# Optimization experiments

Measured on AMD Instinct MI355X. Metric: run time of the kernel, lower is better.

## Reference

```python
import jax, jax.numpy as jnp
import numpy as np

B, T, C = 2, 2048, 1024
N_HEAD = 16
HEAD_DIM = C // N_HEAD


def setup_inputs() -> dict:
    key = jax.random.key(0)
    k1, k2, k3 = jax.random.split(key, 3)
    x = jax.random.normal(k1, (B, T, C), dtype=jnp.float32)
    # weights stored as [in, out]; torch Linear computes x @ W.T with weight [out, in]
    W_qkv = jax.random.normal(k2, (C, 3 * C), dtype=jnp.float32) * (1.0 / np.sqrt(C))
    W_proj = jax.random.normal(k3, (C, C), dtype=jnp.float32) * (1.0 / np.sqrt(C))
    return {"x": x, "W_qkv": W_qkv, "W_proj": W_proj}


def reference(x, W_qkv, W_proj):
    Bb, Tt, Cc = x.shape
    qkv = x @ W_qkv                                # [B,T,3C]
    q, k, v = jnp.split(qkv, 3, axis=2)
    # [B,T,H,D] -> [B,H,T,D]
    q = q.reshape(Bb, Tt, N_HEAD, HEAD_DIM).transpose(0, 2, 1, 3)
    k = k.reshape(Bb, Tt, N_HEAD, HEAD_DIM).transpose(0, 2, 1, 3)
    v = v.reshape(Bb, Tt, N_HEAD, HEAD_DIM).transpose(0, 2, 1, 3)
    scale = 1.0 / np.sqrt(HEAD_DIM).astype(np.float32)
    att = jnp.einsum('bhqd,bhkd->bhqk', q, k) * scale   # [B,H,T,T]
    causal = jnp.tril(jnp.ones((Tt, Tt), dtype=bool))
    att = jnp.where(causal[None, None], att, -jnp.inf)
    att = jax.nn.softmax(att, axis=-1)
    y = jnp.einsum('bhqk,bhkd->bhqd', att, v)           # [B,H,T,D]
    y = y.transpose(0, 2, 1, 3).reshape(Bb, Tt, Cc)
    return y @ W_proj
```

## Files before the change

### kernel.cpp

```cpp
#include <hip/hip_runtime.h>
#include <hip/hip_bf16.h>
#include <math.h>


typedef __bf16 bf16_t;
typedef __bf16 bf16x4 __attribute__((ext_vector_type(4)));
typedef __bf16 bf16x8 __attribute__((ext_vector_type(8)));
typedef float  f32x4  __attribute__((ext_vector_type(4)));
typedef unsigned int u32x4 __attribute__((ext_vector_type(4)));

#define MFMA16(a, b, c) __builtin_amdgcn_mfma_f32_16x16x32_bf16((a), (b), (c), 0, 0, 0)

#define Bn 2
#define Tn 2048
#define Cn 1024
#define Hn 16
#define Dn 64
#define C3 3072
#define Mn 4096
#define QKW 2048
#define NEG_BIG (-1e30f)
#define SCL2 0.18033688011112042f

__device__ __forceinline__ void gload_lds16(const void* g, void* l) {
    __builtin_amdgcn_global_load_lds(
        (const __attribute__((address_space(1))) unsigned int*)g,
        (__attribute__((address_space(3))) unsigned int*)l, 16, 0, 0);
}

__device__ __forceinline__ unsigned cvtpk_bf16(float a, float b) {
    unsigned r;
    asm("v_cvt_pk_bf16_f32 %0, %1, %2" : "=v"(r) : "v"(a), "v"(b));
    return r;
}

__global__ __launch_bounds__(256) void transpose_cvt(const float* __restrict__ in,
                                                     bf16_t* __restrict__ out,
                                                     int K, int N) {
    __shared__ float tile[32][33];
    int n0 = blockIdx.x * 32, k0 = blockIdx.y * 32;
    int tx = threadIdx.x, ty = threadIdx.y;
#pragma unroll
    for (int i = 0; i < 32; i += 8)
        tile[ty + i][tx] = in[(size_t)(k0 + ty + i) * N + n0 + tx];
    __syncthreads();
#pragma unroll
    for (int i = 0; i < 32; i += 8)
        out[(size_t)(n0 + ty + i) * K + k0 + tx] = (bf16_t)tile[tx][ty + i];
}

__global__ __launch_bounds__(256) void cvt_bf16(const float* __restrict__ in,
                                                bf16_t* __restrict__ out) {
    size_t i = ((size_t)blockIdx.x * 256 + threadIdx.x) * 8;
    f32x4 a = *(const f32x4*)(in + i);
    f32x4 b = *(const f32x4*)(in + i + 4);
    bf16x8 r;
    r[0] = (bf16_t)a[0]; r[1] = (bf16_t)a[1]; r[2] = (bf16_t)a[2]; r[3] = (bf16_t)a[3];
    r[4] = (bf16_t)b[0]; r[5] = (bf16_t)b[1]; r[6] = (bf16_t)b[2]; r[7] = (bf16_t)b[3];
    *(bf16x8*)(out + i) = r;
}

template <typename AT, typename CT, int MODE>
__global__ __launch_bounds__(256) void gemm_m97(const AT* __restrict__ A, int lda,
                                                const bf16_t* __restrict__ BT,
                                                CT* __restrict__ Cout, int ldc, int Kd,
                                                bf16_t* __restrict__ qk,
                                                bf16_t* __restrict__ vT) {
    constexpr bool AF32 = (sizeof(AT) == 4);
    __shared__ AT     As[128 * 32];
    __shared__ bf16_t Bs[128 * 32];

    const int tid = threadIdx.x;
    const int w = tid >> 6, lane = tid & 63;
    const int l16 = lane & 15, quad = lane >> 4;
    const int wm = w & 1, wn = w >> 1;
    const int n0 = blockIdx.x * 128;
    const int m0 = blockIdx.y * 128;

    f32x4 zero = {0.f, 0.f, 0.f, 0.f};
    f32x4 acc[4][4];
#pragma unroll
    for (int mb = 0; mb < 4; mb++)
#pragma unroll
        for (int nb = 0; nb < 4; nb++) acc[mb][nb] = zero;

    for (int k = 0; k < Kd; k += 32) {
        __syncthreads();
        if (AF32) {
#pragma unroll
            for (int j = 0; j < 4; j++) {
                int seg = w * 4 + j;
                int r = seg * 8 + (lane >> 3);
                int cc = (lane & 7) ^ (r & 7);
                const float* g = (const float*)A + (size_t)(m0 + r) * lda + k + cc * 4;
                gload_lds16(g, (char*)As + seg * 1024);
            }
        } else {
#pragma unroll
            for (int j = 0; j < 2; j++) {
                int seg = w * 2 + j;
                int r = seg * 16 + (lane >> 2);
                int cc = (lane & 3) ^ (r & 3);
                const bf16_t* g = (const bf16_t*)A + (size_t)(m0 + r) * lda + k + cc * 8;
                gload_lds16(g, (char*)As + seg * 1024);
            }
        }
#pragma unroll
        for (int j = 0; j < 2; j++) {
            int seg = w * 2 + j;
            int r = seg * 16 + (lane >> 2);
            int cc = (lane & 3) ^ (r & 3);
            const bf16_t* g = BT + (size_t)(n0 + r) * Kd + k + cc * 8;
            gload_lds16(g, (char*)Bs + seg * 1024);
        }
        __syncthreads();

        bf16x8 af[4], bf[4];
#pragma unroll
        for (int mb = 0; mb < 4; mb++) {
            int r = wm * 64 + mb * 16 + l16;
            if (AF32) {
                f32x4 x0 = *(const f32x4*)((const char*)As + (r * 8 + ((quad * 2) ^ (r & 7))) * 16);
                f32x4 x1 = *(const f32x4*)((const char*)As + (r * 8 + ((quad * 2 + 1) ^ (r & 7))) * 16);
                bf16x8 t;
                t[0] = (bf16_t)x0[0]; t[1] = (bf16_t)x0[1]; t[2] = (bf16_t)x0[2]; t[3] = (bf16_t)x0[3];
                t[4] = (bf16_t)x1[0]; t[5] = (bf16_t)x1[1]; t[6] = (bf16_t)x1[2]; t[7] = (bf16_t)x1[3];
                af[mb] = t;
            } else {
                af[mb] = *(const bf16x8*)((const char*)As + (r * 4 + (quad ^ (r & 3))) * 16);
            }
        }
#pragma unroll
        for (int nb = 0; nb < 4; nb++) {
            int r = wn * 64 + nb * 16 + l16;
            bf[nb] = *(const bf16x8*)((const char*)Bs + (r * 4 + (quad ^ (r & 3))) * 16);
        }
#pragma unroll
        for (int mb = 0; mb < 4; mb++)
#pragma unroll
            for (int nb = 0; nb < 4; nb++)
                acc[mb][nb] = MFMA16(af[mb], bf[nb], acc[mb][nb]);
    }

#pragma unroll
    for (int mb = 0; mb < 4; mb++)
#pragma unroll
        for (int nb = 0; nb < 4; nb++) {
            const int col = n0 + wn * 64 + nb * 16 + l16;
            const int row0 = m0 + wm * 64 + mb * 16 + quad * 4;
            if (MODE == 0) {
#pragma unroll
                for (int rr = 0; rr < 4; rr++)
                    Cout[(size_t)(row0 + rr) * ldc + col] = (CT)acc[mb][nb][rr];
            } else {
                if (col < 2048) {
                    const float sc = (col < 1024) ? SCL2 : 1.0f;
#pragma unroll
                    for (int rr = 0; rr < 4; rr++)
                        qk[(size_t)(row0 + rr) * QKW + col] = (bf16_t)(acc[mb][nb][rr] * sc);
                } else {
                    int hcol = col - 2048;
                    int bb = row0 >> 11, t0 = row0 & 2047;
                    bf16x4 pv;
#pragma unroll
                    for (int rr = 0; rr < 4; rr++) pv[rr] = (bf16_t)acc[mb][nb][rr];
                    *(bf16x4*)(vT + ((size_t)(bb * 1024 + hcol)) * Tn + t0) = pv;
                }
            }
        }
}

__global__ __launch_bounds__(256) void gemm_s(const bf16_t* __restrict__ A, int lda,
                                              const bf16_t* __restrict__ BT,
                                              float* __restrict__ Cout, int ldc, int Kd) {
    __shared__ bf16_t As[64 * 32];
    __shared__ bf16_t Bs[128 * 32];

    const int tid = threadIdx.x;
    const int w = tid >> 6, lane = tid & 63;
    const int l16 = lane & 15, quad = lane >> 4;
    const int wm = w & 1, wn = w >> 1;
    const int n0 = blockIdx.x * 128;
    const int m0 = blockIdx.y * 64;

    f32x4 zero = {0.f, 0.f, 0.f, 0.f};
    f32x4 acc[2][4];
#pragma unroll
    for (int mb = 0; mb < 2; mb++)
#pragma unroll
        for (int nb = 0; nb < 4; nb++) acc[mb][nb] = zero;

    for (int k = 0; k < Kd; k += 32) {
        __syncthreads();
        {
            int r = w * 16 + (lane >> 2);
            int cc = (lane & 3) ^ (r & 3);
            const bf16_t* g = A + (size_t)(m0 + r) * lda + k + cc * 8;
            gload_lds16(g, (char*)As + w * 1024);
        }
#pragma unroll
        for (int j = 0; j < 2; j++) {
            int seg = w * 2 + j;
            int r = seg * 16 + (lane >> 2);
            int cc = (lane & 3) ^ (r & 3);
            const bf16_t* g = BT + (size_t)(n0 + r) * Kd + k + cc * 8;
            gload_lds16(g, (char*)Bs + seg * 1024);
        }
        __syncthreads();

        bf16x8 af[2], bf[4];
#pragma unroll
        for (int mb = 0; mb < 2; mb++) {
            int r = wm * 32 + mb * 16 + l16;
            af[mb] = *(const bf16x8*)((const char*)As + (r * 4 + (quad ^ (r & 3))) * 16);
        }
#pragma unroll
        for (int nb = 0; nb < 4; nb++) {
            int r = wn * 64 + nb * 16 + l16;
            bf[nb] = *(const bf16x8*)((const char*)Bs + (r * 4 + (quad ^ (r & 3))) * 16);
        }
#pragma unroll
        for (int mb = 0; mb < 2; mb++)
#pragma unroll
            for (int nb = 0; nb < 4; nb++)
                acc[mb][nb] = MFMA16(af[mb], bf[nb], acc[mb][nb]);
    }

#pragma unroll
    for (int mb = 0; mb < 2; mb++)
#pragma unroll
        for (int nb = 0; nb < 4; nb++) {
            const int col = n0 + wn * 64 + nb * 16 + l16;
            const int row0 = m0 + wm * 32 + mb * 16 + quad * 4;
#pragma unroll
            for (int rr = 0; rr < 4; rr++)
                Cout[(size_t)(row0 + rr) * ldc + col] = acc[mb][nb][rr];
        }
}

__global__ __launch_bounds__(256) void attn_kernel(bf16_t* __restrict__ qk,
                                                   const bf16_t* __restrict__ vT) {
    const int id = blockIdx.x;
    const int bh = id & 31;
    const int pr = id >> 5;
    const int b = bh >> 4, h = bh & 15;
    const int tA = pr;
    const int tB = 31 - pr;
    const int tmax = tB;

    const int tid = threadIdx.x;
    const int wave = tid >> 6, lane = tid & 63;
    const int l16 = lane & 15, quad = lane >> 4;

    __shared__ __align__(16) bf16_t Kb[3][64 * 64];
    __shared__ __align__(16) bf16_t Vb[3][64 * 64];

    bf16_t* qbase = qk + (size_t)b * Tn * QKW + h * Dn;
    const bf16_t* kbase = qk + (size_t)b * Tn * QKW + Cn + h * Dn;
    const bf16_t* vbase = vT + (size_t)(b * 1024 + h * Dn) * Tn;

    const int qA = tA * 64 + wave * 16;
    const int qB = tB * 64 + wave * 16;

    bf16x8 qfA[2], qfB[2];
#pragma unroll
    for (int ks = 0; ks < 2; ks++) {
        qfA[ks] = *(const bf16x8*)(qbase + (size_t)(qA + l16) * QKW + ks * 32 + quad * 8);
        qfB[ks] = *(const bf16x8*)(qbase + (size_t)(qB + l16) * QKW + ks * 32 + quad * 8);
    }

    bf16x8 ones;
#pragma unroll
    for (int j = 0; j < 8; j++) ones[j] = (bf16_t)1.0f;

    f32x4 zero = {0.f, 0.f, 0.f, 0.f};
    f32x4 oA[4], oB[4];
    f32x4 olA, olB;
#pragma unroll
    for (int i = 0; i < 4; i++) { oA[i] = zero; oB[i] = zero; }
    olA = zero; olB = zero;

    const int gl = quad >> 1, sub = (quad & 1) * 8;
    int kOff[2][4], vLo[2][4], vHi[2][4];
#pragma unroll
    for (int ks = 0; ks < 2; ks++)
#pragma unroll
        for (int nb = 0; nb < 4; nb++) {
            int R = nb * 16 + l16, r7 = R & 7;
            kOff[ks][nb] = R * 128 + (((ks * 4 + quad) ^ r7) << 4);
            vLo[ks][nb]  = R * 128 + (((ks * 4 + gl) ^ r7) << 4) + sub;
            vHi[ks][nb]  = R * 128 + (((ks * 4 + 2 + gl) ^ r7) << 4) + sub;
        }

    const int r8 = lane >> 3;
    const int cc = (lane & 7) ^ r8;
    auto STAGE = [&](int t, int pg) {
        const int key0 = t * 64;
#pragma unroll
        for (int j = 0; j < 2; j++) {
            int seg = wave * 2 + j;
            gload_lds16(kbase + (size_t)(key0 + seg * 8 + r8) * QKW + cc * 8,
                        (char*)&Kb[pg][0] + seg * 1024);
            gload_lds16(vbase + (size_t)(seg * 8 + r8) * Tn + key0 + cc * 8,
                        (char*)&Vb[pg][0] + seg * 1024);
        }
    };

    STAGE(0, 0);
    STAGE(1, 1);
    int cur = 0;

    for (int t = 0; t <= tmax; ++t) {
        asm volatile("s_waitcnt vmcnt(4)" ::: "memory");
        __builtin_amdgcn_sched_barrier(0);
        __builtin_amdgcn_s_barrier();
        __builtin_amdgcn_sched_barrier(0);
        if (t + 2 <= tmax) {
            int st = cur + 2; if (st >= 3) st -= 3;
            STAGE(t + 2, st);
        }
        __builtin_amdgcn_sched_barrier(0);

        const bool shp = (t <= tA);
        const char* Kc = (const char*)&Kb[cur][0];
        const char* Vc = (const char*)&Vb[cur][0];

        bf16x8 kf[2][4];
#pragma unroll
        for (int ks = 0; ks < 2; ks++)
#pragma unroll
            for (int nbk = 0; nbk < 4; nbk++)
                kf[ks][nbk] = *(const bf16x8*)(Kc + kOff[ks][nbk]);

        bf16x8 pfA[2], pfB[2];

        {
            f32x4 sx[4];
#pragma unroll
            for (int nbk = 0; nbk < 4; nbk++) sx[nbk] = zero;
            __builtin_amdgcn_s_setprio(1);
#pragma unroll
            for (int nbk = 0; nbk < 4; nbk++) {
                sx[nbk] = MFMA16(kf[0][nbk], qfB[0], sx[nbk]);
                sx[nbk] = MFMA16(kf[1][nbk], qfB[1], sx[nbk]);
            }
            __builtin_amdgcn_s_setprio(0);
            if (t == tB) {
                int q = qB + l16;
#pragma unroll
                for (int nbk = 0; nbk < 4; nbk++)
#pragma unroll
                    for (int r = 0; r < 4; r++) {
                        int key = t * 64 + nbk * 16 + quad * 4 + r;
                        if (key > q) sx[nbk][r] = NEG_BIG;
                    }
            }
#pragma unroll
            for (int nbk = 0; nbk < 4; nbk++)
#pragma unroll
                for (int r = 0; r < 4; r++)
                    sx[nbk][r] = __builtin_amdgcn_exp2f(sx[nbk][r]);
#pragma unroll
            for (int ks = 0; ks < 2; ks++) {
                u32x4 wds;
                wds.x = cvtpk_bf16(sx[2 * ks][0], sx[2 * ks][1]);
                wds.y = cvtpk_bf16(sx[2 * ks][2], sx[2 * ks][3]);
                wds.z = cvtpk_bf16(sx[2 * ks + 1][0], sx[2 * ks + 1][1]);
                wds.w = cvtpk_bf16(sx[2 * ks + 1][2], sx[2 * ks + 1][3]);
                pfB[ks] = __builtin_bit_cast(bf16x8, wds);
            }
        }

        if (shp) {
            f32x4 sx[4];
#pragma unroll
            for (int nbk = 0; nbk < 4; nbk++) sx[nbk] = zero;
            __builtin_amdgcn_s_setprio(1);
#pragma unroll
            for (int nbk = 0; nbk < 4; nbk++) {
                sx[nbk] = MFMA16(kf[0][nbk], qfA[0], sx[nbk]);
                sx[nbk] = MFMA16(kf[1][nbk], qfA[1], sx[nbk]);
            }
            __builtin_amdgcn_s_setprio(0);
            if (t == tA) {
                int q = qA + l16;
#pragma unroll
                for (int nbk = 0; nbk < 4; nbk++)
#pragma unroll
                    for (int r = 0; r < 4; r++) {
                        int key = t * 64 + nbk * 16 + quad * 4 + r;
                        if (key > q) sx[nbk][r] = NEG_BIG;
                    }
            }
#pragma unroll
            for (int nbk = 0; nbk < 4; nbk++)
#pragma unroll
                for (int r = 0; r < 4; r++)
                    sx[nbk][r] = __builtin_amdgcn_exp2f(sx[nbk][r]);
#pragma unroll
            for (int ks = 0; ks < 2; ks++) {
                u32x4 wds;
                wds.x = cvtpk_bf16(sx[2 * ks][0], sx[2 * ks][1]);
                wds.y = cvtpk_bf16(sx[2 * ks][2], sx[2 * ks][3]);
                wds.z = cvtpk_bf16(sx[2 * ks + 1][0], sx[2 * ks + 1][1]);
                wds.w = cvtpk_bf16(sx[2 * ks + 1][2], sx[2 * ks + 1][3]);
                pfA[ks] = __builtin_bit_cast(bf16x8, wds);
            }
        } else {
            u32x4 z = {0u, 0u, 0u, 0u};
            pfA[0] = __builtin_bit_cast(bf16x8, z);
            pfA[1] = __builtin_bit_cast(bf16x8, z);
        }

        __builtin_amdgcn_s_setprio(1);
#pragma unroll
        for (int ks = 0; ks < 2; ks++) {
#pragma unroll
            for (int nbd = 0; nbd < 4; nbd++) {
                bf16x4 lo = *(const bf16x4*)(Vc + vLo[ks][nbd]);
                bf16x4 hi = *(const bf16x4*)(Vc + vHi[ks][nbd]);
                bf16x8 vf;
                vf[0] = lo[0]; vf[1] = lo[1]; vf[2] = lo[2]; vf[3] = lo[3];
                vf[4] = hi[0]; vf[5] = hi[1]; vf[6] = hi[2]; vf[7] = hi[3];
                oB[nbd] = MFMA16(pfB[ks], vf, oB[nbd]);
                if (shp) oA[nbd] = MFMA16(pfA[ks], vf, oA[nbd]);
            }
            olB = MFMA16(pfB[ks], ones, olB);
            if (shp) olA = MFMA16(pfA[ks], ones, olA);
        }
        __builtin_amdgcn_s_setprio(0);

        cur = cur + 1; if (cur >= 3) cur -= 3;
    }

#pragma unroll
    for (int nbd = 0; nbd < 4; nbd++)
#pragma unroll
        for (int r = 0; r < 4; r++) {
            int ta = qA + quad * 4 + r;
            int tb = qB + quad * 4 + r;
            qbase[(size_t)ta * QKW + nbd * 16 + l16] = (bf16_t)(oA[nbd][r] / olA[r]);
            qbase[(size_t)tb * QKW + nbd * 16 + l16] = (bf16_t)(oB[nbd][r] / olB[r]);
        }
}

extern "C" void kernel_launch(void* const* d_in, const int* in_sizes, int n_in,
                              void* d_out, int out_size, void* d_ws, size_t ws_size,
                              hipStream_t stream) {
    const float* x     = (const float*)d_in[0];
    const float* Wqkv  = (const float*)d_in[1];
    const float* Wproj = (const float*)d_in[2];
    float* out = (float*)d_out;

    bf16_t* qk     = (bf16_t*)d_ws;
    bf16_t* vT     = qk + (size_t)Mn * QKW;
    bf16_t* wqkvT  = vT + (size_t)QKW * Tn;
    bf16_t* wprojT = wqkvT + (size_t)C3 * Cn;
    bf16_t* xb     = wprojT + (size_t)Cn * Cn;

    const size_t NEED_XB = ((size_t)Mn * QKW + (size_t)QKW * Tn + (size_t)C3 * Cn +
                            (size_t)Cn * Cn + (size_t)Mn * Cn) * sizeof(bf16_t);

    transpose_cvt<<<dim3(C3 / 32, Cn / 32), dim3(32, 8), 0, stream>>>(Wqkv, wqkvT, Cn, C3);
    transpose_cvt<<<dim3(Cn / 32, Cn / 32), dim3(32, 8), 0, stream>>>(Wproj, wprojT, Cn, Cn);

    if (ws_size >= NEED_XB) {
        cvt_bf16<<<dim3((Mn * Cn) / 2048), 256, 0, stream>>>(x, xb);
        gemm_m97<bf16_t, bf16_t, 1><<<dim3(C3 / 128, Mn / 128), 256, 0, stream>>>(
            xb, Cn, wqkvT, (bf16_t*)nullptr, 0, Cn, qk, vT);
    } else {
        gemm_m97<float, bf16_t, 1><<<dim3(C3 / 128, Mn / 128), 256, 0, stream>>>(
            x, Cn, wqkvT, (bf16_t*)nullptr, 0, Cn, qk, vT);
    }
    attn_kernel<<<dim3(512), 256, 0, stream>>>(qk, vT);
    gemm_s<<<dim3(Cn / 128, Mn / 64), 256, 0, stream>>>(qk, QKW, wprojT, out, Cn, Cn);
}
```

Before: 187.5 us.

## Fuse prep kernels, stage V epilogue through LDS, and simplify V fragment loads

```diff
diff --git a/kernel.cpp b/kernel.cpp
--- a/kernel.cpp
+++ b/kernel.cpp
@@ -34,12 +34,35 @@
     return r;
 }
 
-__global__ __launch_bounds__(256) void transpose_cvt(const float* __restrict__ in,
-                                                     bf16_t* __restrict__ out,
-                                                     int K, int N) {
+__global__ __launch_bounds__(256) void prep(const float* __restrict__ Wqkv,
+                                            const float* __restrict__ Wproj,
+                                            const float* __restrict__ x,
+                                            bf16_t* __restrict__ wqkvT,
+                                            bf16_t* __restrict__ wprojT,
+                                            bf16_t* __restrict__ xb) {
     __shared__ float tile[32][33];
-    int n0 = blockIdx.x * 32, k0 = blockIdx.y * 32;
-    int tx = threadIdx.x, ty = threadIdx.y;
+    const int bid = blockIdx.x;
+    const int tid = threadIdx.x;
+    if (bid >= 4096) {
+        size_t i = ((size_t)(bid - 4096) * 256 + tid) * 8;
+        f32x4 a = *(const f32x4*)(x + i);
+        f32x4 b = *(const f32x4*)(x + i + 4);
+        bf16x8 r;
+        r[0] = (bf16_t)a[0]; r[1] = (bf16_t)a[1]; r[2] = (bf16_t)a[2]; r[3] = (bf16_t)a[3];
+        r[4] = (bf16_t)b[0]; r[5] = (bf16_t)b[1]; r[6] = (bf16_t)b[2]; r[7] = (bf16_t)b[3];
+        *(bf16x8*)(xb + i) = r;
+        return;
+    }
+    const float* in; bf16_t* out; int K, N, n0, k0;
+    if (bid < 3072) {
+        in = Wqkv; out = wqkvT; K = Cn; N = C3;
+        n0 = (bid % 96) * 32; k0 = (bid / 96) * 32;
+    } else {
+        int b2 = bid - 3072;
+        in = Wproj; out = wprojT; K = Cn; N = Cn;
+        n0 = (b2 & 31) * 32; k0 = (b2 >> 5) * 32;
+    }
+    const int tx = tid & 31, ty = tid >> 5;
 #pragma unroll
     for (int i = 0; i < 32; i += 8)
         tile[ty + i][tx] = in[(size_t)(k0 + ty + i) * N + n0 + tx];
@@ -47,17 +70,6 @@
 #pragma unroll
     for (int i = 0; i < 32; i += 8)
         out[(size_t)(n0 + ty + i) * K + k0 + tx] = (bf16_t)tile[tx][ty + i];
-}
-
-__global__ __launch_bounds__(256) void cvt_bf16(const float* __restrict__ in,
-                                                bf16_t* __restrict__ out) {
-    size_t i = ((size_t)blockIdx.x * 256 + threadIdx.x) * 8;
-    f32x4 a = *(const f32x4*)(in + i);
-    f32x4 b = *(const f32x4*)(in + i + 4);
-    bf16x8 r;
-    r[0] = (bf16_t)a[0]; r[1] = (bf16_t)a[1]; r[2] = (bf16_t)a[2]; r[3] = (bf16_t)a[3];
-    r[4] = (bf16_t)b[0]; r[5] = (bf16_t)b[1]; r[6] = (bf16_t)b[2]; r[7] = (bf16_t)b[3];
-    *(bf16x8*)(out + i) = r;
 }
 
 template <typename AT, typename CT, int MODE>
@@ -67,8 +79,12 @@
                                                 bf16_t* __restrict__ qk,
                                                 bf16_t* __restrict__ vT) {
     constexpr bool AF32 = (sizeof(AT) == 4);
-    __shared__ AT     As[128 * 32];
-    __shared__ bf16_t Bs[128 * 32];
+    constexpr int SZ_AB = 128 * 32 * (int)sizeof(AT) + 128 * 32 * (int)sizeof(bf16_t);
+    constexpr int SZ_VS = 128 * 136 * (int)sizeof(bf16_t);
+    constexpr int SZ = (MODE == 1 && SZ_VS > SZ_AB) ? SZ_VS : SZ_AB;
+    __shared__ __align__(16) char smem[SZ];
+    AT*     As = (AT*)smem;
+    bf16_t* Bs = (bf16_t*)(smem + 128 * 32 * sizeof(AT));
 
     const int tid = threadIdx.x;
     const int w = tid >> 6, lane = tid & 63;
@@ -142,32 +158,53 @@
                 acc[mb][nb] = MFMA16(af[mb], bf[nb], acc[mb][nb]);
     }
 
-#pragma unroll
-    for (int mb = 0; mb < 4; mb++)
-#pragma unroll
-        for (int nb = 0; nb < 4; nb++) {
-            const int col = n0 + wn * 64 + nb * 16 + l16;
-            const int row0 = m0 + wm * 64 + mb * 16 + quad * 4;
-            if (MODE == 0) {
+    if (MODE == 0) {
+#pragma unroll
+        for (int mb = 0; mb < 4; mb++)
+#pragma unroll
+            for (int nb = 0; nb < 4; nb++) {
+                const int col = n0 + wn * 64 + nb * 16 + l16;
+                const int row0 = m0 + wm * 64 + mb * 16 + quad * 4;
 #pragma unroll
                 for (int rr = 0; rr < 4; rr++)
                     Cout[(size_t)(row0 + rr) * ldc + col] = (CT)acc[mb][nb][rr];
-            } else {
-                if (col < 2048) {
-                    const float sc = (col < 1024) ? SCL2 : 1.0f;
-#pragma unroll
-                    for (int rr = 0; rr < 4; rr++)
-                        qk[(size_t)(row0 + rr) * QKW + col] = (bf16_t)(acc[mb][nb][rr] * sc);
-                } else {
-                    int hcol = col - 2048;
-                    int bb = row0 >> 11, t0 = row0 & 2047;
-                    bf16x4 pv;
-#pragma unroll
-                    for (int rr = 0; rr < 4; rr++) pv[rr] = (bf16_t)acc[mb][nb][rr];
-                    *(bf16x4*)(vT + ((size_t)(bb * 1024 + hcol)) * Tn + t0) = pv;
-                }
-            }
-        }
+            }
+    } else if (n0 < 2048) {
+#pragma unroll
+        for (int mb = 0; mb < 4; mb++)
+#pragma unroll
+            for (int nb = 0; nb < 4; nb++) {
+                const int col = n0 + wn * 64 + nb * 16 + l16;
+                const int row0 = m0 + wm * 64 + mb * 16 + quad * 4;
+                const float sc = (col < 1024) ? SCL2 : 1.0f;
+#pragma unroll
+                for (int rr = 0; rr < 4; rr++)
+                    qk[(size_t)(row0 + rr) * QKW + col] = (bf16_t)(acc[mb][nb][rr] * sc);
+            }
+    } else {
+        __syncthreads();
+        bf16_t* vs = (bf16_t*)smem;
+#pragma unroll
+        for (int mb = 0; mb < 4; mb++)
+#pragma unroll
+            for (int nb = 0; nb < 4; nb++) {
+                int lcol = wn * 64 + nb * 16 + l16;
+                int lrow = wm * 64 + mb * 16 + quad * 4;
+                int lr = (lrow & ~31) | (((lrow >> 2) & 3) << 3) | (((lrow >> 4) & 1) << 2);
+                bf16x4 pv;
+#pragma unroll
+                for (int rr = 0; rr < 4; rr++) pv[rr] = (bf16_t)acc[mb][nb][rr];
+                *(bf16x4*)(vs + lcol * 136 + lr) = pv;
+            }
+        __syncthreads();
+        const int hc = tid >> 1, hf = (tid & 1) * 64;
+        const int bb = m0 >> 11, tb = m0 & 2047;
+        bf16_t* dst = vT + ((size_t)(bb * 1024 + (n0 - 2048) + hc)) * Tn + tb + hf;
+        const bf16_t* src = vs + hc * 136 + hf;
+#pragma unroll
+        for (int j = 0; j < 8; j++)
+            *(bf16x8*)(dst + j * 8) = *(const bf16x8*)(src + j * 8);
+    }
 }
 
 __global__ __launch_bounds__(256) void gemm_s(const bf16_t* __restrict__ A, int lda,
@@ -280,16 +317,14 @@
     for (int i = 0; i < 4; i++) { oA[i] = zero; oB[i] = zero; }
     olA = zero; olB = zero;
 
-    const int gl = quad >> 1, sub = (quad & 1) * 8;
-    int kOff[2][4], vLo[2][4], vHi[2][4];
+    int kOff[2][4], vOff[2][4];
 #pragma unroll
     for (int ks = 0; ks < 2; ks++)
 #pragma unroll
         for (int nb = 0; nb < 4; nb++) {
             int R = nb * 16 + l16, r7 = R & 7;
             kOff[ks][nb] = R * 128 + (((ks * 4 + quad) ^ r7) << 4);
-            vLo[ks][nb]  = R * 128 + (((ks * 4 + gl) ^ r7) << 4) + sub;
-            vHi[ks][nb]  = R * 128 + (((ks * 4 + 2 + gl) ^ r7) << 4) + sub;
+            vOff[ks][nb] = kOff[ks][nb];
         }
 
     const int r8 = lane >> 3;
@@ -417,11 +452,7 @@
         for (int ks = 0; ks < 2; ks++) {
 #pragma unroll
             for (int nbd = 0; nbd < 4; nbd++) {
-                bf16x4 lo = *(const bf16x4*)(Vc + vLo[ks][nbd]);
-                bf16x4 hi = *(const bf16x4*)(Vc + vHi[ks][nbd]);
-                bf16x8 vf;
-                vf[0] = lo[0]; vf[1] = lo[1]; vf[2] = lo[2]; vf[3] = lo[3];
-                vf[4] = hi[0]; vf[5] = hi[1]; vf[6] = hi[2]; vf[7] = hi[3];
+                bf16x8 vf = *(const bf16x8*)(Vc + vOff[ks][nbd]);
                 oB[nbd] = MFMA16(pfB[ks], vf, oB[nbd]);
                 if (shp) oA[nbd] = MFMA16(pfA[ks], vf, oA[nbd]);
             }
@@ -461,14 +492,12 @@
     const size_t NEED_XB = ((size_t)Mn * QKW + (size_t)QKW * Tn + (size_t)C3 * Cn +
                             (size_t)Cn * Cn + (size_t)Mn * Cn) * sizeof(bf16_t);
 
-    transpose_cvt<<<dim3(C3 / 32, Cn / 32), dim3(32, 8), 0, stream>>>(Wqkv, wqkvT, Cn, C3);
-    transpose_cvt<<<dim3(Cn / 32, Cn / 32), dim3(32, 8), 0, stream>>>(Wproj, wprojT, Cn, Cn);
-
     if (ws_size >= NEED_XB) {
-        cvt_bf16<<<dim3((Mn * Cn) / 2048), 256, 0, stream>>>(x, xb);
+        prep<<<dim3(6144), 256, 0, stream>>>(Wqkv, Wproj, x, wqkvT, wprojT, xb);
         gemm_m97<bf16_t, bf16_t, 1><<<dim3(C3 / 128, Mn / 128), 256, 0, stream>>>(
             xb, Cn, wqkvT, (bf16_t*)nullptr, 0, Cn, qk, vT);
     } else {
+        prep<<<dim3(4096), 256, 0, stream>>>(Wqkv, Wproj, x, wqkvT, wprojT, (bf16_t*)nullptr);
         gemm_m97<float, bf16_t, 1><<<dim3(C3 / 128, Mn / 128), 256, 0, stream>>>(
             x, Cn, wqkvT, (bf16_t*)nullptr, 0, Cn, qk, vT);
     }
```

New measurement: 183.3 us. -2.2%, faster.
